# Performance work log

Hardware: AMD Instinct MI355X
Metric: run time of the kernel (lower is better)

Reference implementation:

```python
import jax, jax.numpy as jnp
import numpy as np

NUM_GRAPHS = 512


def setup_inputs() -> dict:
    key = jax.random.key(0)
    k1, k2, k3, k4, k5 = jax.random.split(key, 5)
    N, D = 131072, 512
    x = jax.random.normal(k1, (N, D), dtype=jnp.float32)
    graph_ptr = jnp.sort(jax.random.randint(k2, (N,), 0, NUM_GRAPHS, dtype=jnp.int64))
    # Linear(dim, dim) params (kaiming-ish scale) and query vector
    W = jax.random.normal(k3, (D, D), dtype=jnp.float32) / np.sqrt(D)
    b = jax.random.normal(k4, (D,), dtype=jnp.float32) * 0.01
    query = jax.random.normal(k5, (D,), dtype=jnp.float32)
    return {"x": x, "graph_ptr": graph_ptr, "W": W, "b": b, "query": query}


def reference(x, graph_ptr, W, b, query):
    # gate: Linear + Tanh, then score = g @ query  -> [N]
    g = jnp.tanh(x @ W.T + b)
    score = g @ query
    seg = graph_ptr.astype(jnp.int32)
    # segmented, numerically-stable softmax over nodes of each graph
    seg_max = jax.ops.segment_max(score, seg, num_segments=NUM_GRAPHS)  # [G]
    # empty segments give -inf max; they have no nodes so gather is safe
    e = jnp.exp(score - seg_max[seg])                                   # [N]
    denom = jax.ops.segment_sum(e, seg, num_segments=NUM_GRAPHS)        # [G]
    attn = e / jnp.where(denom[seg] == 0, 1.0, denom[seg])              # [N]
    # weighted scatter-sum of node features per graph -> [G, D]
    out = jax.ops.segment_sum(attn[:, None] * x, seg, num_segments=NUM_GRAPHS)
    return out
```

## Files before the change

kernel.cpp:

```cpp
#include <hip/hip_runtime.h>

typedef _Float16 f16x8 __attribute__((ext_vector_type(8)));
typedef _Float16 f16x4 __attribute__((ext_vector_type(4)));
typedef __fp16 fp16v2 __attribute__((ext_vector_type(2)));
typedef _Float16 f16v2 __attribute__((ext_vector_type(2)));
typedef short short8 __attribute__((ext_vector_type(8)));
typedef float f32x16 __attribute__((ext_vector_type(16)));

#define DD 512
#define NG 512

typedef __attribute__((address_space(3))) void lds_void;
typedef __attribute__((address_space(1))) void glb_void;

static __device__ __forceinline__ void gload_lds16(const void* g, void* l) {
  __builtin_amdgcn_global_load_lds((const glb_void*)g, (lds_void*)l, 16, 0, 0);
}

#define MEMFENCE asm volatile("" ::: "memory")

static __device__ __forceinline__ f16v2 pk16(float a, float b) {
  fp16v2 p = __builtin_amdgcn_cvt_pkrtz(a, b);
  return __builtin_bit_cast(f16v2, p);
}

static __device__ __forceinline__ float fast_tanh(float v) {
  float e = __builtin_amdgcn_exp2f(v * 2.8853900817779268f);
  return 1.0f - 2.0f * __builtin_amdgcn_rcpf(e + 1.0f);
}

__global__ __launch_bounds__(256) void k_convert_w(const float* __restrict__ W,
                                                   unsigned char* __restrict__ Whl) {
  int t = blockIdx.x * 256 + threadIdx.x;
  int r512 = t >> 6, kg = t & 63;
  int ny = r512 >> 8, col = r512 & 255;
  int ct = col >> 5, c31 = col & 31;
  int kt = kg >> 1, khalf = kg & 1;
  const float* p = W + (size_t)r512 * DD + kg * 8;
  short8 h;
#pragma unroll
  for (int j = 0; j < 8; ++j) {
    _Float16 hh = (_Float16)p[j];
    h[j] = (short)__builtin_bit_cast(unsigned short, hh);
  }
  unsigned char* dst = Whl + (size_t)ny * 262144 + (size_t)kt * 8192 +
                       ct * 1024 + (khalf * 32 + c31) * 16;
  *(short8*)dst = h;
}

__global__ __launch_bounds__(256, 2) void k_gemm_score(
    const float* __restrict__ x, const unsigned char* __restrict__ Whl,
    const float* __restrict__ bias, const float* __restrict__ query,
    float* __restrict__ score_part, int N) {
  __shared__ unsigned char ldsB[2][16384];
  __shared__ unsigned char ldsA[2][8192];
  __shared__ float comb[2][128];
  const int tid = threadIdx.x;
  const int wave = tid >> 6;
  const int lane = tid & 63;
  const int l31 = lane & 31;
  const int kh = lane >> 5;
  const int rg = wave >> 1;
  const int cg = wave & 1;
  const int ny = blockIdx.x;
  const int brow0 = blockIdx.y * 128;

  const unsigned char* wsrc = Whl + (size_t)ny * 262144 +
                              (size_t)wave * 2048 + (size_t)lane * 16;

  const float* asrc = x + (size_t)(brow0 + (tid >> 2)) * DD + (tid & 3) * 4;
  const int awoff = ((tid & 3) >> 1) * 2048 + (tid >> 2) * 16 + (tid & 1) * 8;
  const int aroff = kh * 2048 + (rg * 64 + l31) * 16;

  f32x16 acc[2][4];
#pragma unroll
  for (int f = 0; f < 2; ++f)
#pragma unroll
    for (int j = 0; j < 4; ++j)
#pragma unroll
      for (int r = 0; r < 16; ++r) acc[f][j][r] = 0.f;

  float4 aB[4];

#define AISSUE(S)                                                           \
  do {                                                                      \
    _Pragma("unroll")                                                       \
    for (int j = 0; j < 2; ++j)                                             \
      _Pragma("unroll")                                                     \
      for (int c = 0; c < 2; ++c)                                           \
        aB[j * 2 + c] = *(const float4*)(asrc + (size_t)c * 64 * DD +       \
                                         ((2 * (S) + j) & 31) * 16);        \
  } while (0)

#define AWRITE(S)                                                           \
  do {                                                                      \
    unsigned char* base_ = &ldsA[(S) & 1][0];                               \
    _Pragma("unroll")                                                       \
    for (int j = 0; j < 2; ++j)                                             \
      _Pragma("unroll")                                                     \
      for (int c = 0; c < 2; ++c) {                                         \
        const float4 v_ = aB[j * 2 + c];                                    \
        f16v2 lo_ = pk16(v_.x, v_.y);                                       \
        f16v2 hi_ = pk16(v_.z, v_.w);                                       \
        f16x4 w_ = {lo_[0], lo_[1], hi_[0], hi_[1]};                        \
        *(f16x4*)(base_ + j * 4096 + awoff + c * 1024) = w_;                \
      }                                                                     \
  } while (0)

#define BISSUE(S)                                                           \
  do {                                                                      \
    unsigned char* db_ = &ldsB[(S) & 1][wave * 2048];                       \
    _Pragma("unroll")                                                       \
    for (int j = 0; j < 2; ++j) {                                           \
      const unsigned char* sb_ = wsrc + (size_t)((2 * (S) + j) & 31) * 8192;\
      gload_lds16(sb_, db_ + j * 8192);                                     \
      gload_lds16(sb_ + 1024, db_ + j * 8192 + 1024);                       \
    }                                                                       \
  } while (0)

  AISSUE(0);
  MEMFENCE;
  asm volatile("s_waitcnt vmcnt(0)" ::: "memory");
  AWRITE(0);
  MEMFENCE;
  BISSUE(0);
  MEMFENCE;
  AISSUE(1);
  MEMFENCE;

#define BODY(S)                                                             \
  do {                                                                      \
    asm volatile("s_waitcnt vmcnt(4) lgkmcnt(0)" ::: "memory");             \
    __builtin_amdgcn_s_barrier();                                           \
    MEMFENCE;                                                               \
    BISSUE((S) + 1);      \
    MEMFENCE;                                                               \
    const unsigned char* ap_ = &ldsA[(S) & 1][0];                           \
    const unsigned char* bp_ = &ldsB[(S) & 1][cg * 4096 + lane * 16];       \
    __builtin_amdgcn_s_setprio(1);                                          \
    _Pragma("unroll")                                                       \
    for (int j = 0; j < 2; ++j) {                                           \
      f16x8 a0_ = *(const f16x8*)(ap_ + j * 4096 + aroff);                  \
      f16x8 a1_ = *(const f16x8*)(ap_ + j * 4096 + aroff + 512);            \
      const unsigned char* bb_ = bp_ + j * 8192;                            \
      _Pragma("unroll")                                                     \
      for (int t = 0; t < 4; ++t) {                                         \
        f16x8 bh_ = *(const f16x8*)(bb_ + t * 1024);                        \
        acc[0][t] = __builtin_amdgcn_mfma_f32_32x32x16_f16(a0_, bh_, acc[0][t], 0, 0, 0); \
        acc[1][t] = __builtin_amdgcn_mfma_f32_32x32x16_f16(a1_, bh_, acc[1][t], 0, 0, 0); \
      }                                                                     \
    }                                                                       \
    __builtin_amdgcn_s_setprio(0);                                          \
    MEMFENCE;                                                               \
    asm volatile("s_waitcnt vmcnt(4)" ::: "memory");     \
    AWRITE((S) + 1);                                                        \
    MEMFENCE;                                                               \
    AISSUE(((S) + 2) & 15);                                                 \
    MEMFENCE;                                                               \
  } while (0)

  BODY(0);  BODY(1);  BODY(2);  BODY(3);
  BODY(4);  BODY(5);  BODY(6);  BODY(7);
  BODY(8);  BODY(9);  BODY(10); BODY(11);
  BODY(12); BODY(13); BODY(14); BODY(15);

  float sp[2][16];
#pragma unroll
  for (int f = 0; f < 2; ++f)
#pragma unroll
    for (int r = 0; r < 16; ++r) sp[f][r] = 0.f;
#pragma unroll
  for (int j = 0; j < 4; ++j) {
    const int col = ny * 256 + (cg * 4 + j) * 32 + l31;
    const float bb2 = bias[col];
    const float qq = query[col];
#pragma unroll
    for (int f = 0; f < 2; ++f)
#pragma unroll
      for (int r = 0; r < 16; ++r)
        sp[f][r] += fast_tanh(acc[f][j][r] + bb2) * qq;
  }
  __syncthreads();
#pragma unroll
  for (int f = 0; f < 2; ++f)
#pragma unroll
    for (int r = 0; r < 16; ++r) {
      float v = sp[f][r];
      v += __shfl_xor(v, 1);
      v += __shfl_xor(v, 2);
      v += __shfl_xor(v, 4);
      v += __shfl_xor(v, 8);
      v += __shfl_xor(v, 16);
      if (l31 == 0)
        comb[cg][rg * 64 + f * 32 + (r & 3) + 8 * (r >> 2) + 4 * kh] = v;
    }
  __syncthreads();
  if (tid < 128)
    score_part[(size_t)ny * N + brow0 + tid] = comb[0][tid] + comb[1][tid];
}

__global__ __launch_bounds__(256) void k_softmax_out(
    const float* __restrict__ x, const void* __restrict__ segp,
    const float* __restrict__ sp0, const float* __restrict__ sp1,
    float* __restrict__ out, int N) {
  const int g = blockIdx.x;
  const int tid = threadIdx.x;

  const long long probe = ((const long long*)segp)[N / 2 - 1];
  const bool is64 = ((unsigned long long)probe < (unsigned long long)NG);
  const long long* s64 = (const long long*)segp;
  const int* s32 = (const int*)segp;

  int s0, s1;
  {
    int lo = 0, hi = N;
    while (lo < hi) {
      int m = (lo + hi) >> 1;
      long long v = is64 ? s64[m] : (long long)s32[m];
      if (v < (long long)g) lo = m + 1; else hi = m;
    }
    s0 = lo;
    lo = s0; hi = N;
    while (lo < hi) {
      int m = (lo + hi) >> 1;
      long long v = is64 ? s64[m] : (long long)s32[m];
      if (v < (long long)(g + 1)) lo = m + 1; else hi = m;
    }
    s1 = lo;
  }

  __shared__ float red[4];
  __shared__ float wbuf[512];

  float lm = -INFINITY;
  for (int i = s0 + tid; i < s1; i += 256) lm = fmaxf(lm, sp0[i] + sp1[i]);
#pragma unroll
  for (int m = 1; m < 64; m <<= 1) lm = fmaxf(lm, __shfl_xor(lm, m));
  if ((tid & 63) == 0) red[tid >> 6] = lm;
  __syncthreads();
  const float mx = fmaxf(fmaxf(red[0], red[1]), fmaxf(red[2], red[3]));
  __syncthreads();

  float ls = 0.f;
  for (int i = s0 + tid; i < s1; i += 256) ls += expf(sp0[i] + sp1[i] - mx);
#pragma unroll
  for (int m = 1; m < 64; m <<= 1) ls += __shfl_xor(ls, m);
  if ((tid & 63) == 0) red[tid >> 6] = ls;
  __syncthreads();
  const float sum = red[0] + red[1] + red[2] + red[3];
  const float inv = sum > 0.f ? 1.0f / sum : 0.f;

  float a0 = 0.f, a1 = 0.f;
  const int c = tid * 2;
  for (int base = s0; base < s1; base += 512) {
    const int cnt = min(512, s1 - base);
    __syncthreads();
    for (int i = tid; i < cnt; i += 256)
      wbuf[i] = expf(sp0[base + i] + sp1[base + i] - mx) * inv;
    __syncthreads();
#pragma unroll 8
    for (int j = 0; j < cnt; ++j) {
      const float w = wbuf[j];
      const float2 xv = *(const float2*)(x + (size_t)(base + j) * DD + c);
      a0 = fmaf(w, xv.x, a0);
      a1 = fmaf(w, xv.y, a1);
    }
  }
  float* op = out + (size_t)g * DD + c;
  op[0] = a0;
  op[1] = a1;
}

extern "C" void kernel_launch(void* const* d_in, const int* in_sizes, int n_in,
                              void* d_out, int out_size, void* d_ws, size_t ws_size,
                              hipStream_t stream) {
  const float* x = (const float*)d_in[0];
  const void* seg = d_in[1];
  const float* W = (const float*)d_in[2];
  const float* b = (const float*)d_in[3];
  const float* q = (const float*)d_in[4];
  float* out = (float*)d_out;
  const int N = in_sizes[0] / DD;

  unsigned char* Whl = (unsigned char*)d_ws;
  float* sp0 = (float*)(Whl + 524288);
  float* sp1 = sp0 + N;

  k_convert_w<<<128, 256, 0, stream>>>(W, Whl);
  dim3 grid(2, N / 128);
  k_gemm_score<<<grid, 256, 0, stream>>>(x, Whl, b, q, sp0, N);
  k_softmax_out<<<NG, 256, 0, stream>>>(x, seg, sp0, sp1, out, N);
}
```

Measured before the change: 171.3 us.

## Load W tiles directly into registers instead of staging through LDS

The B operand (converted W) is now read from global memory straight into VGPRs, with a two-deep register double buffer, instead of being copied into LDS via global_load_lds and read back. This removes the LDS B buffer and its LDS read traffic and may raise occupancy. In exchange each wave issues its own global loads (column-group waves duplicate loads that were shared through LDS before), uses more VGPRs, and relies on compiler-inserted vmcnt waits, since the explicit ones were removed.

```diff
diff --git a/kernel.cpp b/kernel.cpp
--- a/kernel.cpp
+++ b/kernel.cpp
@@ -9,13 +9,6 @@
 
 #define DD 512
 #define NG 512
-
-typedef __attribute__((address_space(3))) void lds_void;
-typedef __attribute__((address_space(1))) void glb_void;
-
-static __device__ __forceinline__ void gload_lds16(const void* g, void* l) {
-  __builtin_amdgcn_global_load_lds((const glb_void*)g, (lds_void*)l, 16, 0, 0);
-}
 
 #define MEMFENCE asm volatile("" ::: "memory")
 
@@ -52,7 +45,6 @@
     const float* __restrict__ x, const unsigned char* __restrict__ Whl,
     const float* __restrict__ bias, const float* __restrict__ query,
     float* __restrict__ score_part, int N) {
-  __shared__ unsigned char ldsB[2][16384];
   __shared__ unsigned char ldsA[2][8192];
   __shared__ float comb[2][128];
   const int tid = threadIdx.x;
@@ -65,8 +57,8 @@
   const int ny = blockIdx.x;
   const int brow0 = blockIdx.y * 128;
 
-  const unsigned char* wsrc = Whl + (size_t)ny * 262144 +
-                              (size_t)wave * 2048 + (size_t)lane * 16;
+  const unsigned char* bsrc = Whl + (size_t)ny * 262144 + cg * 4096 +
+                              (size_t)lane * 16;
 
   const float* asrc = x + (size_t)(brow0 + (tid >> 2)) * DD + (tid & 3) * 4;
   const int awoff = ((tid & 3) >> 1) * 2048 + (tid >> 2) * 16 + (tid & 1) * 8;
@@ -81,6 +73,7 @@
       for (int r = 0; r < 16; ++r) acc[f][j][r] = 0.f;
 
   float4 aB[4];
+  f16x8 b0[4], b1[4];
 
 #define AISSUE(S)                                                           \
   do {                                                                      \
@@ -107,52 +100,52 @@
       }                                                                     \
   } while (0)
 
-#define BISSUE(S)                                                           \
-  do {                                                                      \
-    unsigned char* db_ = &ldsB[(S) & 1][wave * 2048];                       \
-    _Pragma("unroll")                                                       \
-    for (int j = 0; j < 2; ++j) {                                           \
-      const unsigned char* sb_ = wsrc + (size_t)((2 * (S) + j) & 31) * 8192;\
-      gload_lds16(sb_, db_ + j * 8192);                                     \
-      gload_lds16(sb_ + 1024, db_ + j * 8192 + 1024);                       \
+#define BLOAD(KT, R)                                                        \
+  do {                                                                      \
+    const unsigned char* sb_ = bsrc + (size_t)((KT) & 31) * 8192;           \
+    _Pragma("unroll")                                                       \
+    for (int t = 0; t < 4; ++t)                                             \
+      R[t] = *(const f16x8*)(sb_ + t * 1024);                               \
+  } while (0)
+
+#define MFMA_HALF(AP, J2, B)                                                \
+  do {                                                                      \
+    f16x8 a0_ = *(const f16x8*)((AP) + (J2) * 4096 + aroff);                \
+    f16x8 a1_ = *(const f16x8*)((AP) + (J2) * 4096 + aroff + 512);          \
+    _Pragma("unroll")                                                       \
+    for (int t = 0; t < 4; ++t) {                                           \
+      acc[0][t] = __builtin_amdgcn_mfma_f32_32x32x16_f16(a0_, B[t], acc[0][t], 0, 0, 0); \
+      acc[1][t] = __builtin_amdgcn_mfma_f32_32x32x16_f16(a1_, B[t], acc[1][t], 0, 0, 0); \
     }                                                                       \
   } while (0)
 
   AISSUE(0);
   MEMFENCE;
-  asm volatile("s_waitcnt vmcnt(0)" ::: "memory");
   AWRITE(0);
   MEMFENCE;
-  BISSUE(0);
+  BLOAD(0, b0);
   MEMFENCE;
   AISSUE(1);
   MEMFENCE;
 
 #define BODY(S)                                                             \
   do {                                                                      \
-    asm volatile("s_waitcnt vmcnt(4) lgkmcnt(0)" ::: "memory");             \
+    asm volatile("s_waitcnt lgkmcnt(0)" ::: "memory");                      \
     __builtin_amdgcn_s_barrier();                                           \
     MEMFENCE;                                                               \
-    BISSUE((S) + 1);      \
+    BLOAD(2 * (S) + 1, b1);                                                 \
     MEMFENCE;                                                               \
     const unsigned char* ap_ = &ldsA[(S) & 1][0];                           \
-    const unsigned char* bp_ = &ldsB[(S) & 1][cg * 4096 + lane * 16];       \
     __builtin_amdgcn_s_setprio(1);                                          \
-    _Pragma("unroll")                                                       \
-    for (int j = 0; j < 2; ++j) {                                           \
-      f16x8 a0_ = *(const f16x8*)(ap_ + j * 4096 + aroff);                  \
-      f16x8 a1_ = *(const f16x8*)(ap_ + j * 4096 + aroff + 512);            \
-      const unsigned char* bb_ = bp_ + j * 8192;                            \
-      _Pragma("unroll")                                                     \
-      for (int t = 0; t < 4; ++t) {                                         \
-        f16x8 bh_ = *(const f16x8*)(bb_ + t * 1024);                        \
-        acc[0][t] = __builtin_amdgcn_mfma_f32_32x32x16_f16(a0_, bh_, acc[0][t], 0, 0, 0); \
-        acc[1][t] = __builtin_amdgcn_mfma_f32_32x32x16_f16(a1_, bh_, acc[1][t], 0, 0, 0); \
-      }                                                                     \
-    }                                                                       \
+    MFMA_HALF(ap_, 0, b0);                                                  \
     __builtin_amdgcn_s_setprio(0);                                          \
     MEMFENCE;                                                               \
-    asm volatile("s_waitcnt vmcnt(4)" ::: "memory");     \
+    BLOAD(2 * (S) + 2, b0);                                                 \
+    MEMFENCE;                                                               \
+    __builtin_amdgcn_s_setprio(1);                                          \
+    MFMA_HALF(ap_, 1, b1);                                                  \
+    __builtin_amdgcn_s_setprio(0);                                          \
+    MEMFENCE;                                                               \
     AWRITE((S) + 1);                                                        \
     MEMFENCE;                                                               \
     AISSUE(((S) + 2) & 15);                                                 \
```

Result: faster. 162.4 us (-5.2%).
